# Kernel optimization log

Measured on AMD Instinct MI355X. Metric: run time of the kernel, lower is better.

The kernel has to match this reference:

```python
import jax, jax.numpy as jnp
import numpy as np
import math

B, L, N, DIM, H = 2, 8, 1024, 512, 8
DH = DIM // H

def setup_inputs() -> dict:
    key = jax.random.key(0)
    ks = jax.random.split(key, 9)
    s = 1.0 / math.sqrt(DIM)
    return {
        "x": jax.random.normal(ks[0], (B, L, N, DIM), dtype=jnp.float32),
        "Wq": jax.random.normal(ks[1], (DIM, DIM), dtype=jnp.float32) * s,
        "bq": jnp.zeros((DIM,), dtype=jnp.float32),
        "Wk": jax.random.normal(ks[2], (DIM, DIM), dtype=jnp.float32) * s,
        "bk": jnp.zeros((DIM,), dtype=jnp.float32),
        "Wv": jax.random.normal(ks[3], (DIM, DIM), dtype=jnp.float32) * s,
        "bv": jnp.zeros((DIM,), dtype=jnp.float32),
        "Wo": jax.random.normal(ks[4], (DIM, DIM), dtype=jnp.float32) * s,
        "bo": jnp.zeros((DIM,), dtype=jnp.float32),
    }

def _split_heads(t):
    # 'b l n (h d) -> b l h n d'
    b, l, n, _ = t.shape
    return t.reshape(b, l, n, H, DH).transpose(0, 1, 3, 2, 4)

def reference(x, Wq, bq, Wk, bk, Wv, bv, Wo, bo):
    q = _split_heads(x @ Wq.T + bq)
    # FAITHFUL BUG: source maps (q, v, k) -> (q_mat, k_mat, v_mat),
    # so the "keys" come from the v projection and "values" from the k projection.
    k_mat = _split_heads(x @ Wv.T + bv)
    v_mat = _split_heads(x @ Wk.T + bk)
    # scale is sqrt(Dh * num_heads) = sqrt(dim), as in the source
    scores = jnp.einsum('blhnd,blhmd->blhnm', q, k_mat) / math.sqrt(DIM)
    weights = jax.nn.softmax(scores, axis=-1)
    inter = jnp.einsum('blhnm,blhmd->blhnd', weights, v_mat)
    # 'b l h n d -> b l n (h d)'
    inter = inter.transpose(0, 1, 3, 2, 4).reshape(x.shape[0], x.shape[1], x.shape[2], DIM)
    return inter @ Wo.T + bo
```

## Files before the change

### kernel.cpp

```cpp
#include <hip/hip_runtime.h>
#include <stdint.h>

#define DIMC 512
#define NSEQ 1024
#define BLT  16
#define NHEAD 8
#define DHD  64
#define MTOT (BLT*NSEQ)

typedef float f32x4 __attribute__((ext_vector_type(4)));
typedef float f32x16 __attribute__((ext_vector_type(16)));
typedef short s16x8 __attribute__((ext_vector_type(8)));
typedef short s16x4 __attribute__((ext_vector_type(4)));

__device__ __forceinline__ unsigned short f2bf(float f) {
    unsigned int u = __float_as_uint(f);
    u += 0x7fffu + ((u >> 16) & 1u);
    return (unsigned short)(u >> 16);
}
__device__ __forceinline__ float bf2f(unsigned short h) {
    return __uint_as_float(((unsigned int)h) << 16);
}

#define QSCALE (0.04419417382415922f * 1.4426950408889634f)

__device__ __forceinline__ void gll16(const void* g, void* l) {
    __builtin_amdgcn_global_load_lds(
        (const __attribute__((address_space(1))) void*)g,
        (__attribute__((address_space(3))) void*)l, 16, 0, 0);
}

__device__ __forceinline__ unsigned int cvtpk(float lo, float hi) {
    unsigned int r;
    asm("v_cvt_pk_bf16_f32 %0, %1, %2" : "=v"(r) : "v"(lo), "v"(hi));
    return r;
}

__device__ __forceinline__ void pl32swap(unsigned int &a, unsigned int &b) {
    asm volatile("v_permlane32_swap_b32 %0, %1" : "+v"(a), "+v"(b));
}

__device__ __forceinline__ bool detect_bf16(const unsigned short* x) {
    int t = threadIdx.x & 63;
    unsigned short v = x[2 * t];
    int e = (v >> 7) & 0xFF;
    unsigned long long ball = __ballot(e < 100 || e > 137);
    return __popcll(ball) < 16;
}

struct ConvArgs {
    const void* src[9];
    unsigned short* dst[9];
};

__global__ __launch_bounds__(256) void conv_kernel(ConvArgs a,
                                                   const unsigned short* __restrict__ xdet) {
    const bool isbf = detect_bf16(xdet);
    int b = blockIdx.x;
    int seg, idx;
    if (b < 4096)      { seg = 0; idx = (b * 256 + threadIdx.x) * 8; }
    else if (b < 4608) { int t = b - 4096; seg = 1 + (t >> 7);
                         idx = (((t & 127) * 256) + threadIdx.x) * 8; }
    else               { int i = threadIdx.x * 8; seg = 5 + (i >> 9); idx = i & 511; }
    const void* s = a.src[seg];
    unsigned short* d = a.dst[seg];
    if (isbf) {
        *(uint4*)(d + idx) = *(const uint4*)((const unsigned short*)s + idx);
    } else {
        float4 t0 = *(const float4*)((const float*)s + idx);
        float4 t1 = *(const float4*)((const float*)s + idx + 4);
        ushort4 v0{f2bf(t0.x), f2bf(t0.y), f2bf(t0.z), f2bf(t0.w)};
        ushort4 v1{f2bf(t1.x), f2bf(t1.y), f2bf(t1.z), f2bf(t1.w)};
        *(ushort4*)(d + idx)     = v0;
        *(ushort4*)(d + idx + 4) = v1;
    }
}

__global__ __launch_bounds__(512) void proj_kernel(
    const unsigned short* __restrict__ xb,
    const unsigned short* __restrict__ Wqb, const unsigned short* __restrict__ Wkb,
    const unsigned short* __restrict__ Wvb,
    const unsigned short* __restrict__ bqb, const unsigned short* __restrict__ bkb,
    const unsigned short* __restrict__ bvb,
    unsigned short* __restrict__ Q, unsigned short* __restrict__ K,
    unsigned short* __restrict__ Vt)
{
    const int bid = blockIdx.x;
    const int xcd = bid & 7;
    const int s = bid >> 3;
    const int z = s >> 5;
    const int r = s & 31;
    const int mt = ((r >> 2) << 3) + xcd;
    const int nt = r & 3;
    const int mBase = mt * 256;
    const int nBase = nt * 128;

    const unsigned short* Wp = (z == 0) ? Wqb : ((z == 1) ? Wvb : Wkb);
    const unsigned short* bp = (z == 0) ? bqb : ((z == 1) ? bvb : bkb);
    unsigned short* outp = (z == 0) ? Q : ((z == 1) ? K : Vt);
    const float oscale = (z == 0) ? QSCALE : 1.0f;

    const int tid = threadIdx.x;
    const int wave = tid >> 6;
    const int lane = tid & 63;
    const int lr = lane & 15, lg = lane >> 4;
    const int wm = wave >> 1, wn = wave & 1;

    __shared__ unsigned short Al[256 * 64];
    __shared__ unsigned short Bl[128 * 64];

    f32x4 acc[4][4];
    #pragma unroll
    for (int a = 0; a < 4; ++a)
        #pragma unroll
        for (int b = 0; b < 4; ++b) acc[a][b] = (f32x4){0.f, 0.f, 0.f, 0.f};

    const int srow = lane >> 3;
    const int scol = (lane & 7) * 8;

    for (int k0 = 0; k0 < DIMC; k0 += 64) {
        #pragma unroll
        for (int i = 0; i < 4; ++i) {
            int row = wave * 32 + i * 8;
            gll16(xb + (long)(mBase + row + srow) * DIMC + k0 + scol, Al + row * 64);
        }
        #pragma unroll
        for (int i = 0; i < 2; ++i) {
            int row = wave * 16 + i * 8;
            gll16(Wp + (long)(nBase + row + srow) * DIMC + k0 + scol, Bl + row * 64);
        }
        __syncthreads();

        #pragma unroll
        for (int kk = 0; kk < 64; kk += 32) {
            s16x8 af[4], bf_[4];
            #pragma unroll
            for (int a = 0; a < 4; ++a)
                af[a] = *(const s16x8*)&Al[(wm * 64 + a * 16 + lr) * 64 + kk + lg * 8];
            #pragma unroll
            for (int b = 0; b < 4; ++b)
                bf_[b] = *(const s16x8*)&Bl[(wn * 64 + b * 16 + lr) * 64 + kk + lg * 8];
            #pragma unroll
            for (int a = 0; a < 4; ++a)
                #pragma unroll
                for (int b = 0; b < 4; ++b)
                    acc[a][b] = __builtin_amdgcn_mfma_f32_16x16x32_bf16(af[a], bf_[b], acc[a][b], 0, 0, 0);
        }
        __syncthreads();
    }

    #pragma unroll
    for (int b = 0; b < 4; ++b) {
        int j = nBase + wn * 64 + b * 16 + lr;
        float bb = bf2f(bp[j]);
        int h = j >> 6, d = j & 63;
        #pragma unroll
        for (int a = 0; a < 4; ++a) {
            int m0 = mBase + wm * 64 + a * 16 + lg * 4;
            int bl = m0 >> 10, n0 = m0 & 1023;
            if (z == 2) {
                ushort4 pk;
                unsigned short* p = (unsigned short*)&pk;
                #pragma unroll
                for (int r2 = 0; r2 < 4; ++r2) p[r2] = f2bf(acc[a][b][r2] + bb);
                int base = (((bl << 3) + h) << 16) + ((n0 >> 5) << 11)
                         + (((n0 >> 3) & 3) << 9) + (d << 3) + (n0 & 7);
                *(ushort4*)&outp[base] = pk;
            } else {
                #pragma unroll
                for (int r2 = 0; r2 < 4; ++r2) {
                    float v = (acc[a][b][r2] + bb) * oscale;
                    outp[(((bl << 3) + h) << 16) + ((n0 + r2) << 6) + d] = f2bf(v);
                }
            }
        }
    }
}

__device__ __forceinline__ void gemm_core_async(
    const unsigned short* __restrict__ Ap, const unsigned short* __restrict__ Wp,
    int mBase, int nBase, unsigned short* Al, unsigned short* Bl, f32x4 acc[4][4])
{
    const int wave = threadIdx.x >> 6;
    const int lane = threadIdx.x & 63;
    const int lr = lane & 15, lg = lane >> 4;
    const int wm = wave >> 1, wn = wave & 1;
    const int srow = lane >> 3;
    const int scol = (lane & 7) * 8;

    #pragma unroll
    for (int a = 0; a < 4; ++a)
        #pragma unroll
        for (int b = 0; b < 4; ++b) acc[a][b] = (f32x4){0.f, 0.f, 0.f, 0.f};

    for (int k0 = 0; k0 < DIMC; k0 += 64) {
        #pragma unroll
        for (int i = 0; i < 4; ++i) {
            int rbase = (wave * 4 + i) * 8;
            gll16(Ap + (long)(mBase + rbase + srow) * DIMC + k0 + scol, Al + rbase * 64);
            gll16(Wp + (long)(nBase + rbase + srow) * DIMC + k0 + scol, Bl + rbase * 64);
        }
        __syncthreads();

        #pragma unroll
        for (int kk = 0; kk < 64; kk += 32) {
            s16x8 af[4], bf_[4];
            #pragma unroll
            for (int a = 0; a < 4; ++a)
                af[a] = *(const s16x8*)&Al[(wm * 64 + a * 16 + lr) * 64 + kk + lg * 8];
            #pragma unroll
            for (int b = 0; b < 4; ++b)
                bf_[b] = *(const s16x8*)&Bl[(wn * 64 + b * 16 + lr) * 64 + kk + lg * 8];
            #pragma unroll
            for (int a = 0; a < 4; ++a)
                #pragma unroll
                for (int b = 0; b < 4; ++b)
                    acc[a][b] = __builtin_amdgcn_mfma_f32_16x16x32_bf16(af[a], bf_[b], acc[a][b], 0, 0, 0);
        }
        __syncthreads();
    }
}

__global__ __launch_bounds__(256) void out_gemm_kernel(
    const unsigned short* __restrict__ inter, const unsigned short* __restrict__ Wob,
    const unsigned short* __restrict__ bob, void* __restrict__ outp,
    const unsigned short* __restrict__ xdet)
{
    const bool isbf = detect_bf16(xdet);
    const int bid = blockIdx.x;
    const int xcd = bid & 7;
    const int s = bid >> 3;
    const int mt = ((s >> 2) << 3) + xcd;
    const int nt = s & 3;

    const int mBase = mt * 128;
    const int nBase = nt * 128;
    const int lane = threadIdx.x & 63;
    const int lr = lane & 15, lg = lane >> 4;
    const int wm = (threadIdx.x >> 6) >> 1, wn = (threadIdx.x >> 6) & 1;

    __shared__ unsigned short Al[128 * 64];
    __shared__ unsigned short Bl[128 * 64];
    f32x4 acc[4][4];
    gemm_core_async(inter, Wob, mBase, nBase, Al, Bl, acc);

    #pragma unroll
    for (int b = 0; b < 4; ++b) {
        int j = nBase + wn * 64 + b * 16 + lr;
        float bb = bf2f(bob[j]);
        #pragma unroll
        for (int a = 0; a < 4; ++a) {
            #pragma unroll
            for (int r = 0; r < 4; ++r) {
                long m = mBase + wm * 64 + a * 16 + lg * 4 + r;
                float v = acc[a][b][r] + bb;
                if (isbf) ((unsigned short*)outp)[m * DIMC + j] = f2bf(v);
                else      ((float*)outp)[m * DIMC + j] = v;
            }
        }
    }
}

#define SWZ(row, col) ((row) * 64 + ((col) ^ (((row) & 7) * 8)))

__global__ __launch_bounds__(256, 3) void attn_kernel(
    const unsigned short* __restrict__ Q, const unsigned short* __restrict__ K,
    const unsigned short* __restrict__ Vt, unsigned short* __restrict__ inter)
{
    const int b = blockIdx.x;
    const int bh = b & 127;
    const int qt = b >> 7;
    const int tid = threadIdx.x;
    const int wave = tid >> 6;
    const int lane = tid & 63;
    const int l31 = lane & 31;
    const int hi = lane >> 5;

    const unsigned short* Qb = Q + (long)bh * (NSEQ * DHD);
    const int qbase = qt * 128 + wave * 32;

    s16x8 qf[4];
    #pragma unroll
    for (int k16 = 0; k16 < 4; ++k16)
        qf[k16] = *(const s16x8*)&Qb[(qbase + l31) * DHD + k16 * 16 + hi * 8];

    __shared__ unsigned short Kl[2][64 * 64];
    __shared__ unsigned short Vl[2][64 * 64];

    const int srow = tid >> 3;
    const int scol = ((tid & 7) * 8) ^ ((srow & 7) * 8);
    const unsigned short* kp = K  + (long)bh * (NSEQ * DHD) + srow * DHD + scol;
    const unsigned short* vg = Vt + (long)bh * (NSEQ * DHD);

    auto stage = [&](int buf, int kt) {
        unsigned short* Kb_ = &Kl[buf][0];
        unsigned short* Vb_ = &Vl[buf][0];
        const long ko = (long)kt * 4096;
        gll16(kp + ko,                                Kb_ + wave * 512);
        gll16(kp + ko + 2048,                         Kb_ + wave * 512 + 2048);
        gll16(vg + ko + wave * 512 + lane * 8,        Vb_ + wave * 512);
        gll16(vg + ko + 2048 + wave * 512 + lane * 8, Vb_ + wave * 512 + 2048);
    };

    f32x16 o[2];
    f32x16 lacc;
    f32x16 zero16;
    #pragma unroll
    for (int r = 0; r < 16; ++r) { o[0][r] = 0.f; o[1][r] = 0.f; lacc[r] = 0.f; zero16[r] = 0.f; }
    const s16x8 ones8 = {(short)0x3F80, (short)0x3F80, (short)0x3F80, (short)0x3F80,
                         (short)0x3F80, (short)0x3F80, (short)0x3F80, (short)0x3F80};

    stage(0, 0);
    __syncthreads();

    #pragma unroll 2
    for (int kt = 0; kt < 16; ++kt) {
        const int cur = kt & 1;
        if (kt < 15)
            stage(cur ^ 1, kt + 1);

        const unsigned short* Kc = &Kl[cur][0];
        const unsigned short* Vc = &Vl[cur][0];

        #pragma unroll
        for (int kc = 0; kc < 2; ++kc) {
            s16x8 af[4];
            #pragma unroll
            for (int k16 = 0; k16 < 4; ++k16)
                af[k16] = *(const s16x8*)&Kc[SWZ(kc * 32 + l31, k16 * 16 + hi * 8)];
            f32x16 s;
            __builtin_amdgcn_s_setprio(1);
            s = __builtin_amdgcn_mfma_f32_32x32x16_bf16(af[0], qf[0], zero16, 0, 0, 0);
            s = __builtin_amdgcn_mfma_f32_32x32x16_bf16(af[1], qf[1], s, 0, 0, 0);
            s = __builtin_amdgcn_mfma_f32_32x32x16_bf16(af[2], qf[2], s, 0, 0, 0);
            s = __builtin_amdgcn_mfma_f32_32x32x16_bf16(af[3], qf[3], s, 0, 0, 0);
            __builtin_amdgcn_s_setprio(0);

            float p[16];
            #pragma unroll
            for (int r = 0; r < 16; ++r) p[r] = __builtin_exp2f(s[r]);
            unsigned int w[4][2];
            #pragma unroll
            for (int b4 = 0; b4 < 4; ++b4) {
                w[b4][0] = cvtpk(p[4 * b4 + 0], p[4 * b4 + 1]);
                w[b4][1] = cvtpk(p[4 * b4 + 2], p[4 * b4 + 3]);
            }
            s16x8 frag[2];
            #pragma unroll
            for (int t16 = 0; t16 < 2; ++t16) {
                unsigned int a0 = w[2 * t16][0], b0 = w[2 * t16 + 1][0];
                unsigned int a1 = w[2 * t16][1], b1 = w[2 * t16 + 1][1];
                pl32swap(a0, b0);
                pl32swap(a1, b1);
                union { unsigned int u[4]; s16x8 v; } f;
                f.u[0] = a0; f.u[1] = a1; f.u[2] = b0; f.u[3] = b1;
                frag[t16] = f.v;
            }

            s16x8 va[2][2];
            #pragma unroll
            for (int dt = 0; dt < 2; ++dt)
                #pragma unroll
                for (int t16 = 0; t16 < 2; ++t16)
                    va[dt][t16] = *(const s16x8*)&Vc[kc * 2048 + (t16 * 2 + hi) * 512
                                                     + (dt * 32 + l31) * 8];
            __builtin_amdgcn_s_setprio(1);
            lacc = __builtin_amdgcn_mfma_f32_32x32x16_bf16(ones8, frag[0], lacc, 0, 0, 0);
            lacc = __builtin_amdgcn_mfma_f32_32x32x16_bf16(ones8, frag[1], lacc, 0, 0, 0);
            #pragma unroll
            for (int dt = 0; dt < 2; ++dt)
                #pragma unroll
                for (int t16 = 0; t16 < 2; ++t16)
                    o[dt] = __builtin_amdgcn_mfma_f32_32x32x16_bf16(va[dt][t16], frag[t16], o[dt], 0, 0, 0);
            __builtin_amdgcn_s_setprio(0);
        }

        if (kt < 15) __syncthreads();
    }

    const int bl = bh >> 3, h = bh & 7;
    const int q = qbase + l31;
    float inv = 1.f / lacc[0];
    #pragma unroll
    for (int dt = 0; dt < 2; ++dt) {
        #pragma unroll
        for (int b4 = 0; b4 < 4; ++b4) {
            unsigned int w0 = cvtpk(o[dt][4 * b4 + 0] * inv, o[dt][4 * b4 + 1] * inv);
            unsigned int w1 = cvtpk(o[dt][4 * b4 + 2] * inv, o[dt][4 * b4 + 3] * inv);
            union { unsigned int u[2]; ushort4 v; } pk;
            pk.u[0] = w0; pk.u[1] = w1;
            *(ushort4*)&inter[((long)(bl * NSEQ + q)) * DIMC + h * 64 + dt * 32 + 8 * b4 + 4 * hi] = pk.v;
        }
    }
}

extern "C" void kernel_launch(void* const* d_in, const int* in_sizes, int n_in,
                              void* d_out, int out_size, void* d_ws, size_t ws_size,
                              hipStream_t stream) {
    const void* x  = d_in[0];
    const void* Wq = d_in[1]; const void* bq = d_in[2];
    const void* Wk = d_in[3]; const void* bk = d_in[4];
    const void* Wv = d_in[5]; const void* bv = d_in[6];
    const void* Wo = d_in[7]; const void* bo = d_in[8];

    char* ws = (char*)d_ws;
    unsigned short* xb  = (unsigned short*)ws;
    unsigned short* Q   = xb + (long)MTOT * DIMC;
    unsigned short* K   = Q  + (long)MTOT * DIMC;
    unsigned short* Vt  = K  + (long)MTOT * DIMC;
    unsigned short* Wqb = Vt + (long)MTOT * DIMC;
    unsigned short* Wkb = Wqb + DIMC * DIMC;
    unsigned short* Wvb = Wkb + DIMC * DIMC;
    unsigned short* Wob = Wvb + DIMC * DIMC;
    unsigned short* bqb = Wob + DIMC * DIMC;
    unsigned short* bkb = bqb + DIMC;
    unsigned short* bvb = bkb + DIMC;
    unsigned short* bob = bvb + DIMC;

    ConvArgs ca;
    ca.src[0] = x;  ca.src[1] = Wq; ca.src[2] = Wk; ca.src[3] = Wv; ca.src[4] = Wo;
    ca.src[5] = bq; ca.src[6] = bk; ca.src[7] = bv; ca.src[8] = bo;
    ca.dst[0] = xb;  ca.dst[1] = Wqb; ca.dst[2] = Wkb; ca.dst[3] = Wvb; ca.dst[4] = Wob;
    ca.dst[5] = bqb; ca.dst[6] = bkb; ca.dst[7] = bvb; ca.dst[8] = bob;
    conv_kernel<<<4609, 256, 0, stream>>>(ca, (const unsigned short*)x);

    proj_kernel<<<768, 512, 0, stream>>>(xb, Wqb, Wkb, Wvb, bqb, bkb, bvb, Q, K, Vt);

    attn_kernel<<<8 * 128, 256, 0, stream>>>(Q, K, Vt, xb );

    out_gemm_kernel<<<512, 256, 0, stream>>>(xb , Wob, bob, d_out,
                                             (const unsigned short*)x);
}
```

Baseline: 209.8 us.

## Fuse fp32-to-bf16 input conversion into projection and output GEMM loads

Removes the separate conversion kernel and converts fp32 x and weights to bf16 while staging them into shared memory inside the projection and output GEMMs. The projection kernel also changes from 256x128 tiles with 512 threads to 128x128 tiles with 256 threads and twice as many blocks. This drops a full read and write pass over x plus one kernel launch. In exchange, the fp32 path uses synchronous register loads with conversion instead of async global-to-LDS copies, and each weight tile is reconverted by every block that reads it.

```diff
diff --git a/kernel.cpp b/kernel.cpp
--- a/kernel.cpp
+++ b/kernel.cpp
@@ -48,86 +48,79 @@
     return __popcll(ball) < 16;
 }
 
-struct ConvArgs {
-    const void* src[9];
-    unsigned short* dst[9];
-};
-
-__global__ __launch_bounds__(256) void conv_kernel(ConvArgs a,
-                                                   const unsigned short* __restrict__ xdet) {
-    const bool isbf = detect_bf16(xdet);
-    int b = blockIdx.x;
-    int seg, idx;
-    if (b < 4096)      { seg = 0; idx = (b * 256 + threadIdx.x) * 8; }
-    else if (b < 4608) { int t = b - 4096; seg = 1 + (t >> 7);
-                         idx = (((t & 127) * 256) + threadIdx.x) * 8; }
-    else               { int i = threadIdx.x * 8; seg = 5 + (i >> 9); idx = i & 511; }
-    const void* s = a.src[seg];
-    unsigned short* d = a.dst[seg];
-    if (isbf) {
-        *(uint4*)(d + idx) = *(const uint4*)((const unsigned short*)s + idx);
-    } else {
-        float4 t0 = *(const float4*)((const float*)s + idx);
-        float4 t1 = *(const float4*)((const float*)s + idx + 4);
-        ushort4 v0{f2bf(t0.x), f2bf(t0.y), f2bf(t0.z), f2bf(t0.w)};
-        ushort4 v1{f2bf(t1.x), f2bf(t1.y), f2bf(t1.z), f2bf(t1.w)};
-        *(ushort4*)(d + idx)     = v0;
-        *(ushort4*)(d + idx + 4) = v1;
-    }
-}
-
-__global__ __launch_bounds__(512) void proj_kernel(
-    const unsigned short* __restrict__ xb,
-    const unsigned short* __restrict__ Wqb, const unsigned short* __restrict__ Wkb,
-    const unsigned short* __restrict__ Wvb,
-    const unsigned short* __restrict__ bqb, const unsigned short* __restrict__ bkb,
-    const unsigned short* __restrict__ bvb,
+__global__ __launch_bounds__(256) void proj_kernel(
+    const void* __restrict__ xr,
+    const void* __restrict__ Wqr, const void* __restrict__ Wkr,
+    const void* __restrict__ Wvr,
+    const void* __restrict__ bqr, const void* __restrict__ bkr,
+    const void* __restrict__ bvr,
     unsigned short* __restrict__ Q, unsigned short* __restrict__ K,
     unsigned short* __restrict__ Vt)
 {
+    const bool isbf = detect_bf16((const unsigned short*)xr);
     const int bid = blockIdx.x;
     const int xcd = bid & 7;
     const int s = bid >> 3;
-    const int z = s >> 5;
-    const int r = s & 31;
+    const int z = s >> 6;
+    const int r = s & 63;
     const int mt = ((r >> 2) << 3) + xcd;
     const int nt = r & 3;
-    const int mBase = mt * 256;
-    const int nBase = nt * 128;
-
-    const unsigned short* Wp = (z == 0) ? Wqb : ((z == 1) ? Wvb : Wkb);
-    const unsigned short* bp = (z == 0) ? bqb : ((z == 1) ? bvb : bkb);
+
+    const void* Wr = (z == 0) ? Wqr : ((z == 1) ? Wvr : Wkr);
+    const void* br = (z == 0) ? bqr : ((z == 1) ? bvr : bkr);
     unsigned short* outp = (z == 0) ? Q : ((z == 1) ? K : Vt);
     const float oscale = (z == 0) ? QSCALE : 1.0f;
 
+    const int mBase = mt * 128;
+    const int nBase = nt * 128;
     const int tid = threadIdx.x;
     const int wave = tid >> 6;
     const int lane = tid & 63;
     const int lr = lane & 15, lg = lane >> 4;
     const int wm = wave >> 1, wn = wave & 1;
-
-    __shared__ unsigned short Al[256 * 64];
-    __shared__ unsigned short Bl[128 * 64];
-
-    f32x4 acc[4][4];
-    #pragma unroll
-    for (int a = 0; a < 4; ++a)
-        #pragma unroll
-        for (int b = 0; b < 4; ++b) acc[a][b] = (f32x4){0.f, 0.f, 0.f, 0.f};
-
     const int srow = lane >> 3;
     const int scol = (lane & 7) * 8;
 
+    __shared__ unsigned short Al[128 * 64];
+    __shared__ unsigned short Bl[128 * 64];
+
+    f32x4 acc[4][4];
+    #pragma unroll
+    for (int a = 0; a < 4; ++a)
+        #pragma unroll
+        for (int b = 0; b < 4; ++b) acc[a][b] = (f32x4){0.f, 0.f, 0.f, 0.f};
+
     for (int k0 = 0; k0 < DIMC; k0 += 64) {
-        #pragma unroll
-        for (int i = 0; i < 4; ++i) {
-            int row = wave * 32 + i * 8;
-            gll16(xb + (long)(mBase + row + srow) * DIMC + k0 + scol, Al + row * 64);
-        }
-        #pragma unroll
-        for (int i = 0; i < 2; ++i) {
-            int row = wave * 16 + i * 8;
-            gll16(Wp + (long)(nBase + row + srow) * DIMC + k0 + scol, Bl + row * 64);
+        if (isbf) {
+            const unsigned short* xu = (const unsigned short*)xr;
+            const unsigned short* Wu = (const unsigned short*)Wr;
+            #pragma unroll
+            for (int i = 0; i < 4; ++i) {
+                int rbase = (wave * 4 + i) * 8;
+                gll16(xu + (long)(mBase + rbase + srow) * DIMC + k0 + scol, Al + rbase * 64);
+                gll16(Wu + (long)(nBase + rbase + srow) * DIMC + k0 + scol, Bl + rbase * 64);
+            }
+        } else {
+            const float* xf = (const float*)xr;
+            const float* Wf = (const float*)Wr;
+            #pragma unroll
+            for (int i = 0; i < 4; ++i) {
+                int row = (wave * 4 + i) * 8 + srow;
+                const float* ap = xf + (long)(mBase + row) * DIMC + k0 + scol;
+                float4 a0 = *(const float4*)ap;
+                float4 a1 = *(const float4*)(ap + 4);
+                uint4 pa;
+                pa.x = cvtpk(a0.x, a0.y); pa.y = cvtpk(a0.z, a0.w);
+                pa.z = cvtpk(a1.x, a1.y); pa.w = cvtpk(a1.z, a1.w);
+                *(uint4*)&Al[row * 64 + scol] = pa;
+                const float* wp_ = Wf + (long)(nBase + row) * DIMC + k0 + scol;
+                float4 b0 = *(const float4*)wp_;
+                float4 b1 = *(const float4*)(wp_ + 4);
+                uint4 pb;
+                pb.x = cvtpk(b0.x, b0.y); pb.y = cvtpk(b0.z, b0.w);
+                pb.z = cvtpk(b1.x, b1.y); pb.w = cvtpk(b1.z, b1.w);
+                *(uint4*)&Bl[row * 64 + scol] = pb;
+            }
         }
         __syncthreads();
 
@@ -152,7 +145,7 @@
     #pragma unroll
     for (int b = 0; b < 4; ++b) {
         int j = nBase + wn * 64 + b * 16 + lr;
-        float bb = bf2f(bp[j]);
+        float bb = isbf ? bf2f(((const unsigned short*)br)[j]) : ((const float*)br)[j];
         int h = j >> 6, d = j & 63;
         #pragma unroll
         for (int a = 0; a < 4; ++a) {
@@ -177,53 +170,9 @@
     }
 }
 
-__device__ __forceinline__ void gemm_core_async(
-    const unsigned short* __restrict__ Ap, const unsigned short* __restrict__ Wp,
-    int mBase, int nBase, unsigned short* Al, unsigned short* Bl, f32x4 acc[4][4])
-{
-    const int wave = threadIdx.x >> 6;
-    const int lane = threadIdx.x & 63;
-    const int lr = lane & 15, lg = lane >> 4;
-    const int wm = wave >> 1, wn = wave & 1;
-    const int srow = lane >> 3;
-    const int scol = (lane & 7) * 8;
-
-    #pragma unroll
-    for (int a = 0; a < 4; ++a)
-        #pragma unroll
-        for (int b = 0; b < 4; ++b) acc[a][b] = (f32x4){0.f, 0.f, 0.f, 0.f};
-
-    for (int k0 = 0; k0 < DIMC; k0 += 64) {
-        #pragma unroll
-        for (int i = 0; i < 4; ++i) {
-            int rbase = (wave * 4 + i) * 8;
-            gll16(Ap + (long)(mBase + rbase + srow) * DIMC + k0 + scol, Al + rbase * 64);
-            gll16(Wp + (long)(nBase + rbase + srow) * DIMC + k0 + scol, Bl + rbase * 64);
-        }
-        __syncthreads();
-
-        #pragma unroll
-        for (int kk = 0; kk < 64; kk += 32) {
-            s16x8 af[4], bf_[4];
-            #pragma unroll
-            for (int a = 0; a < 4; ++a)
-                af[a] = *(const s16x8*)&Al[(wm * 64 + a * 16 + lr) * 64 + kk + lg * 8];
-            #pragma unroll
-            for (int b = 0; b < 4; ++b)
-                bf_[b] = *(const s16x8*)&Bl[(wn * 64 + b * 16 + lr) * 64 + kk + lg * 8];
-            #pragma unroll
-            for (int a = 0; a < 4; ++a)
-                #pragma unroll
-                for (int b = 0; b < 4; ++b)
-                    acc[a][b] = __builtin_amdgcn_mfma_f32_16x16x32_bf16(af[a], bf_[b], acc[a][b], 0, 0, 0);
-        }
-        __syncthreads();
-    }
-}
-
 __global__ __launch_bounds__(256) void out_gemm_kernel(
-    const unsigned short* __restrict__ inter, const unsigned short* __restrict__ Wob,
-    const unsigned short* __restrict__ bob, void* __restrict__ outp,
+    const unsigned short* __restrict__ inter, const void* __restrict__ Wor,
+    const void* __restrict__ bor, void* __restrict__ outp,
     const unsigned short* __restrict__ xdet)
 {
     const bool isbf = detect_bf16(xdet);
@@ -235,19 +184,74 @@
 
     const int mBase = mt * 128;
     const int nBase = nt * 128;
-    const int lane = threadIdx.x & 63;
+    const int tid = threadIdx.x;
+    const int wave = tid >> 6;
+    const int lane = tid & 63;
     const int lr = lane & 15, lg = lane >> 4;
-    const int wm = (threadIdx.x >> 6) >> 1, wn = (threadIdx.x >> 6) & 1;
+    const int wm = wave >> 1, wn = wave & 1;
+    const int srow = lane >> 3;
+    const int scol = (lane & 7) * 8;
 
     __shared__ unsigned short Al[128 * 64];
     __shared__ unsigned short Bl[128 * 64];
+
     f32x4 acc[4][4];
-    gemm_core_async(inter, Wob, mBase, nBase, Al, Bl, acc);
+    #pragma unroll
+    for (int a = 0; a < 4; ++a)
+        #pragma unroll
+        for (int b = 0; b < 4; ++b) acc[a][b] = (f32x4){0.f, 0.f, 0.f, 0.f};
+
+    for (int k0 = 0; k0 < DIMC; k0 += 64) {
+        #pragma unroll
+        for (int i = 0; i < 4; ++i) {
+            int rbase = (wave * 4 + i) * 8;
+            gll16(inter + (long)(mBase + rbase + srow) * DIMC + k0 + scol, Al + rbase * 64);
+        }
+        if (isbf) {
+            const unsigned short* Wu = (const unsigned short*)Wor;
+            #pragma unroll
+            for (int i = 0; i < 4; ++i) {
+                int rbase = (wave * 4 + i) * 8;
+                gll16(Wu + (long)(nBase + rbase + srow) * DIMC + k0 + scol, Bl + rbase * 64);
+            }
+        } else {
+            const float* Wf = (const float*)Wor;
+            #pragma unroll
+            for (int i = 0; i < 4; ++i) {
+                int row = (wave * 4 + i) * 8 + srow;
+                const float* wp_ = Wf + (long)(nBase + row) * DIMC + k0 + scol;
+                float4 b0 = *(const float4*)wp_;
+                float4 b1 = *(const float4*)(wp_ + 4);
+                uint4 pb;
+                pb.x = cvtpk(b0.x, b0.y); pb.y = cvtpk(b0.z, b0.w);
+                pb.z = cvtpk(b1.x, b1.y); pb.w = cvtpk(b1.z, b1.w);
+                *(uint4*)&Bl[row * 64 + scol] = pb;
+            }
+        }
+        __syncthreads();
+
+        #pragma unroll
+        for (int kk = 0; kk < 64; kk += 32) {
+            s16x8 af[4], bf_[4];
+            #pragma unroll
+            for (int a = 0; a < 4; ++a)
+                af[a] = *(const s16x8*)&Al[(wm * 64 + a * 16 + lr) * 64 + kk + lg * 8];
+            #pragma unroll
+            for (int b = 0; b < 4; ++b)
+                bf_[b] = *(const s16x8*)&Bl[(wn * 64 + b * 16 + lr) * 64 + kk + lg * 8];
+            #pragma unroll
+            for (int a = 0; a < 4; ++a)
+                #pragma unroll
+                for (int b = 0; b < 4; ++b)
+                    acc[a][b] = __builtin_amdgcn_mfma_f32_16x16x32_bf16(af[a], bf_[b], acc[a][b], 0, 0, 0);
+        }
+        __syncthreads();
+    }
 
     #pragma unroll
     for (int b = 0; b < 4; ++b) {
         int j = nBase + wn * 64 + b * 16 + lr;
-        float bb = bf2f(bob[j]);
+        float bb = isbf ? bf2f(((const unsigned short*)bor)[j]) : ((const float*)bor)[j];
         #pragma unroll
         for (int a = 0; a < 4; ++a) {
             #pragma unroll
@@ -404,30 +408,15 @@
     const void* Wo = d_in[7]; const void* bo = d_in[8];
 
     char* ws = (char*)d_ws;
-    unsigned short* xb  = (unsigned short*)ws;
-    unsigned short* Q   = xb + (long)MTOT * DIMC;
+    unsigned short* inter = (unsigned short*)ws;
+    unsigned short* Q   = inter + (long)MTOT * DIMC;
     unsigned short* K   = Q  + (long)MTOT * DIMC;
     unsigned short* Vt  = K  + (long)MTOT * DIMC;
-    unsigned short* Wqb = Vt + (long)MTOT * DIMC;
-    unsigned short* Wkb = Wqb + DIMC * DIMC;
-    unsigned short* Wvb = Wkb + DIMC * DIMC;
-    unsigned short* Wob = Wvb + DIMC * DIMC;
-    unsigned short* bqb = Wob + DIMC * DIMC;
-    unsigned short* bkb = bqb + DIMC;
-    unsigned short* bvb = bkb + DIMC;
-    unsigned short* bob = bvb + DIMC;
-
-    ConvArgs ca;
-    ca.src[0] = x;  ca.src[1] = Wq; ca.src[2] = Wk; ca.src[3] = Wv; ca.src[4] = Wo;
-    ca.src[5] = bq; ca.src[6] = bk; ca.src[7] = bv; ca.src[8] = bo;
-    ca.dst[0] = xb;  ca.dst[1] = Wqb; ca.dst[2] = Wkb; ca.dst[3] = Wvb; ca.dst[4] = Wob;
-    ca.dst[5] = bqb; ca.dst[6] = bkb; ca.dst[7] = bvb; ca.dst[8] = bob;
-    conv_kernel<<<4609, 256, 0, stream>>>(ca, (const unsigned short*)x);
-
-    proj_kernel<<<768, 512, 0, stream>>>(xb, Wqb, Wkb, Wvb, bqb, bkb, bvb, Q, K, Vt);
-
-    attn_kernel<<<8 * 128, 256, 0, stream>>>(Q, K, Vt, xb );
-
-    out_gemm_kernel<<<512, 256, 0, stream>>>(xb , Wob, bob, d_out,
+
+    proj_kernel<<<1536, 256, 0, stream>>>(x, Wq, Wk, Wv, bq, bk, bv, Q, K, Vt);
+
+    attn_kernel<<<8 * 128, 256, 0, stream>>>(Q, K, Vt, inter);
+
+    out_gemm_kernel<<<512, 256, 0, stream>>>(inter, Wo, bo, d_out,
                                              (const unsigned short*)x);
 }
```

After: 225.4 us. +7.4%, slower.

## Double-buffer LDS tiles in QKV projection GEMM with K-step of 32

Applied to the files above, without the earlier changes.

Changes the QKV projection GEMM main loop from single-buffered 64-wide K tiles to double-buffered 32-wide tiles. The next tile's global-to-LDS load is issued before computing on the current one, so memory latency can overlap with MFMA work. LDS footprint stays the same, but there are twice as many iterations, each with less compute to hide load latency. It also relies on a single barrier per iteration, whose correctness depends on how the async LDS loads are ordered.

```diff
diff --git a/kernel.cpp b/kernel.cpp
--- a/kernel.cpp
+++ b/kernel.cpp
@@ -106,8 +106,11 @@
     const int lr = lane & 15, lg = lane >> 4;
     const int wm = wave >> 1, wn = wave & 1;
 
-    __shared__ unsigned short Al[256 * 64];
-    __shared__ unsigned short Bl[128 * 64];
+    const int srow = lane >> 2;
+    const int scol = (lane & 3) * 8;
+
+    __shared__ unsigned short Al[2 * 256 * 32];
+    __shared__ unsigned short Bl[2 * 128 * 32];
 
     f32x4 acc[4][4];
     #pragma unroll
@@ -115,38 +118,41 @@
         #pragma unroll
         for (int b = 0; b < 4; ++b) acc[a][b] = (f32x4){0.f, 0.f, 0.f, 0.f};
 
-    const int srow = lane >> 3;
-    const int scol = (lane & 7) * 8;
-
-    for (int k0 = 0; k0 < DIMC; k0 += 64) {
-        #pragma unroll
-        for (int i = 0; i < 4; ++i) {
-            int row = wave * 32 + i * 8;
-            gll16(xb + (long)(mBase + row + srow) * DIMC + k0 + scol, Al + row * 64);
-        }
-        #pragma unroll
-        for (int i = 0; i < 2; ++i) {
-            int row = wave * 16 + i * 8;
-            gll16(Wp + (long)(nBase + row + srow) * DIMC + k0 + scol, Bl + row * 64);
-        }
-        __syncthreads();
-
-        #pragma unroll
-        for (int kk = 0; kk < 64; kk += 32) {
-            s16x8 af[4], bf_[4];
-            #pragma unroll
-            for (int a = 0; a < 4; ++a)
-                af[a] = *(const s16x8*)&Al[(wm * 64 + a * 16 + lr) * 64 + kk + lg * 8];
+    auto stage = [&](int buf, int k0) {
+        unsigned short* Ab = Al + buf * 8192;
+        unsigned short* Bb = Bl + buf * 4096;
+        gll16(xb + (long)(mBase + wave * 32 + srow) * DIMC + k0 + scol,
+              Ab + wave * 1024);
+        gll16(xb + (long)(mBase + wave * 32 + 16 + srow) * DIMC + k0 + scol,
+              Ab + wave * 1024 + 512);
+        gll16(Wp + (long)(nBase + wave * 16 + srow) * DIMC + k0 + scol,
+              Bb + wave * 512);
+    };
+
+    stage(0, 0);
+    __syncthreads();
+
+    #pragma unroll 2
+    for (int k = 0; k < 16; ++k) {
+        const int cur = k & 1;
+        if (k < 15) stage(cur ^ 1, (k + 1) * 32);
+
+        const unsigned short* Ac = Al + cur * 8192;
+        const unsigned short* Bc = Bl + cur * 4096;
+        s16x8 af[4], bf_[4];
+        #pragma unroll
+        for (int a = 0; a < 4; ++a)
+            af[a] = *(const s16x8*)&Ac[(wm * 64 + a * 16 + lr) * 32 + lg * 8];
+        #pragma unroll
+        for (int b = 0; b < 4; ++b)
+            bf_[b] = *(const s16x8*)&Bc[(wn * 64 + b * 16 + lr) * 32 + lg * 8];
+        #pragma unroll
+        for (int a = 0; a < 4; ++a)
             #pragma unroll
             for (int b = 0; b < 4; ++b)
-                bf_[b] = *(const s16x8*)&Bl[(wn * 64 + b * 16 + lr) * 64 + kk + lg * 8];
-            #pragma unroll
-            for (int a = 0; a < 4; ++a)
-                #pragma unroll
-                for (int b = 0; b < 4; ++b)
-                    acc[a][b] = __builtin_amdgcn_mfma_f32_16x16x32_bf16(af[a], bf_[b], acc[a][b], 0, 0, 0);
-        }
-        __syncthreads();
+                acc[a][b] = __builtin_amdgcn_mfma_f32_16x16x32_bf16(af[a], bf_[b], acc[a][b], 0, 0, 0);
+
+        if (k < 15) __syncthreads();
     }
 
     #pragma unroll
```

Result: no change. 207.1 us (median of 3 runs) (-1.3%).
